# Kernel optimization log

Hardware: AMD Instinct MI355X
Metric: run time of the kernel (lower is better)

## Reference

```python
import jax, jax.numpy as jnp
import numpy as np

N_S, N_T, E, B = 100000, 100000, 2000000, 10000
F_XS, F_XT, F_E, F_U = 10, 5, 10, 10


def setup_inputs() -> dict:
    key = jax.random.key(0)
    ks = jax.random.split(key, 8)
    return {
        "x_s": jax.random.normal(ks[0], (N_S, F_XS), dtype=jnp.float32),
        "x_t": jax.random.normal(ks[1], (N_T, F_XT), dtype=jnp.float32),
        "edge_index": jax.random.randint(ks[2], (2, E), 0, N_S),
        "edge_attr": jax.random.normal(ks[3], (E, F_E), dtype=jnp.float32),
        "u": jax.random.normal(ks[4], (B, F_U), dtype=jnp.float32),
        "batch_e": jax.random.randint(ks[5], (E,), 0, B),
        "W1": jax.random.normal(ks[6], (F_XS + F_XT + F_E + F_U, F_E), dtype=jnp.float32) * (1.0 / np.sqrt(F_XS + F_XT + F_E + F_U)),
        "b1": jnp.zeros((F_E,), dtype=jnp.float32),
        "W2": jax.random.normal(ks[7], (F_E, F_E), dtype=jnp.float32) * (1.0 / np.sqrt(F_E)),
        "b2": jnp.zeros((F_E,), dtype=jnp.float32),
    }


def reference(x_s, x_t, edge_index, edge_attr, u, batch_e, W1, b1, W2, b2):
    src, tgt = edge_index[0], edge_index[1]
    # Gather + concat: [E, F_xs + F_xt + F_e + F_u]
    h = jnp.concatenate([x_s[src], x_t[tgt], edge_attr, u[batch_e]], axis=-1)
    h = jax.nn.leaky_relu(h @ W1 + b1, negative_slope=0.1)
    return h @ W2 + b2  # [E, F_e]
```

## Files before the change

kernel.cpp:

```cpp
#include <hip/hip_runtime.h>


#define F_XS 10
#define F_XT 5
#define F_E  10
#define F_U  10
#define F_IN 35

__global__ __launch_bounds__(256) void edge_model_kernel(
    const float* __restrict__ x_s,
    const float* __restrict__ x_t,
    const int*   __restrict__ edge_index,
    const float* __restrict__ edge_attr,
    const float* __restrict__ u,
    const int*   __restrict__ batch_e,
    const float* __restrict__ W1,
    const float* __restrict__ b1,
    const float* __restrict__ W2,
    const float* __restrict__ b2,
    float*       __restrict__ out,
    int E)
{
    const int e = blockIdx.x * blockDim.x + threadIdx.x;
    if (e >= E) return;

    const int src = edge_index[e];
    const int tgt = edge_index[E + e];
    const int be  = batch_e[e];

    float in[F_IN];

    {
        const float2* p = (const float2*)(x_s + (long long)src * F_XS);
        #pragma unroll
        for (int i = 0; i < 5; ++i) { float2 v = p[i]; in[2*i] = v.x; in[2*i+1] = v.y; }
    }
    {
        const float* p = x_t + (long long)tgt * F_XT;
        #pragma unroll
        for (int i = 0; i < 5; ++i) in[10 + i] = p[i];
    }
    {
        const float2* p = (const float2*)(edge_attr + (long long)e * F_E);
        #pragma unroll
        for (int i = 0; i < 5; ++i) { float2 v = p[i]; in[15 + 2*i] = v.x; in[16 + 2*i] = v.y; }
    }
    {
        const float2* p = (const float2*)(u + (long long)be * F_U);
        #pragma unroll
        for (int i = 0; i < 5; ++i) { float2 v = p[i]; in[25 + 2*i] = v.x; in[26 + 2*i] = v.y; }
    }

    float h[F_E];
    #pragma unroll
    for (int j = 0; j < F_E; ++j) h[j] = b1[j];
    #pragma unroll
    for (int k = 0; k < F_IN; ++k) {
        const float a = in[k];
        #pragma unroll
        for (int j = 0; j < F_E; ++j) h[j] = fmaf(a, W1[k * F_E + j], h[j]);
    }
    #pragma unroll
    for (int j = 0; j < F_E; ++j) h[j] = (h[j] >= 0.0f) ? h[j] : 0.1f * h[j];

    float o[F_E];
    #pragma unroll
    for (int j = 0; j < F_E; ++j) o[j] = b2[j];
    #pragma unroll
    for (int k = 0; k < F_E; ++k) {
        const float a = h[k];
        #pragma unroll
        for (int j = 0; j < F_E; ++j) o[j] = fmaf(a, W2[k * F_E + j], o[j]);
    }

    float2* po = (float2*)(out + (long long)e * F_E);
    #pragma unroll
    for (int i = 0; i < 5; ++i) {
        float2 v; v.x = o[2*i]; v.y = o[2*i + 1];
        po[i] = v;
    }
}

extern "C" void kernel_launch(void* const* d_in, const int* in_sizes, int n_in,
                              void* d_out, int out_size, void* d_ws, size_t ws_size,
                              hipStream_t stream) {
    const float* x_s        = (const float*)d_in[0];
    const float* x_t        = (const float*)d_in[1];
    const int*   edge_index = (const int*)  d_in[2];
    const float* edge_attr  = (const float*)d_in[3];
    const float* u          = (const float*)d_in[4];
    const int*   batch_e    = (const int*)  d_in[5];
    const float* W1         = (const float*)d_in[6];
    const float* b1         = (const float*)d_in[7];
    const float* W2         = (const float*)d_in[8];
    const float* b2         = (const float*)d_in[9];
    float*       out        = (float*)d_out;

    const int E = in_sizes[5];
    const int block = 256;
    const int grid  = (E + block - 1) / block;

    edge_model_kernel<<<grid, block, 0, stream>>>(
        x_s, x_t, edge_index, edge_attr, u, batch_e, W1, b1, W2, b2, out, E);
}
```

Measured before the change: 248.9 us.

## Process two edges per thread with wide vector gathers and nontemporal streaming

Each thread now handles a pair of adjacent edges. Index loads become int2, node and global-feature rows are gathered with float4/float2 loads, and edge_attr and the output use 16-byte nontemporal loads and stores since the pair's 80-byte span is aligned. The aim is fewer, wider memory transactions, more loads in flight per thread, and less cache pollution from streamed data. In exchange, register pressure roughly doubles, and float4 loads on 20- and 40-byte row strides rely on the hardware tolerating unaligned vector accesses.

New measurement: 276.1 us. 1.11x slower.

```diff
diff --git a/kernel.cpp b/kernel.cpp
--- a/kernel.cpp
+++ b/kernel.cpp
@@ -6,6 +6,50 @@
 #define F_E  10
 #define F_U  10
 #define F_IN 35
+
+typedef float vf4 __attribute__((ext_vector_type(4)));
+union F4 { vf4 v; float f[4]; };
+
+__device__ __forceinline__ void gather10(const float* __restrict__ p, float* __restrict__ dst) {
+    float4 a = *(const float4*)(p);
+    float4 b = *(const float4*)(p + 4);
+    float2 c = *(const float2*)(p + 8);
+    dst[0]=a.x; dst[1]=a.y; dst[2]=a.z; dst[3]=a.w;
+    dst[4]=b.x; dst[5]=b.y; dst[6]=b.z; dst[7]=b.w;
+    dst[8]=c.x; dst[9]=c.y;
+}
+
+__device__ __forceinline__ void gather5(const float* __restrict__ p, float* __restrict__ dst) {
+    float4 a = *(const float4*)(p);
+    dst[0]=a.x; dst[1]=a.y; dst[2]=a.z; dst[3]=a.w;
+    dst[4]=p[4];
+}
+
+__device__ __forceinline__ void mlp(const float* __restrict__ in,
+                                    const float* __restrict__ W1, const float* __restrict__ b1,
+                                    const float* __restrict__ W2, const float* __restrict__ b2,
+                                    float* __restrict__ o) {
+    float h[F_E];
+    #pragma unroll
+    for (int j = 0; j < F_E; ++j) h[j] = b1[j];
+    #pragma unroll
+    for (int k = 0; k < F_IN; ++k) {
+        const float a = in[k];
+        #pragma unroll
+        for (int j = 0; j < F_E; ++j) h[j] = fmaf(a, W1[k * F_E + j], h[j]);
+    }
+    #pragma unroll
+    for (int j = 0; j < F_E; ++j) h[j] = (h[j] >= 0.0f) ? h[j] : 0.1f * h[j];
+
+    #pragma unroll
+    for (int j = 0; j < F_E; ++j) o[j] = b2[j];
+    #pragma unroll
+    for (int k = 0; k < F_E; ++k) {
+        const float a = h[k];
+        #pragma unroll
+        for (int j = 0; j < F_E; ++j) o[j] = fmaf(a, W2[k * F_E + j], o[j]);
+    }
+}
 
 __global__ __launch_bounds__(256) void edge_model_kernel(
     const float* __restrict__ x_s,
@@ -21,63 +65,62 @@
     float*       __restrict__ out,
     int E)
 {
-    const int e = blockIdx.x * blockDim.x + threadIdx.x;
-    if (e >= E) return;
+    const int t  = blockIdx.x * blockDim.x + threadIdx.x;
+    const int e0 = 2 * t;
+    if (e0 >= E) return;
+    const bool two = (e0 + 1) < E;
 
-    const int src = edge_index[e];
-    const int tgt = edge_index[E + e];
-    const int be  = batch_e[e];
+    const int2 sp = *(const int2*)(edge_index + e0);
+    const int2 tp = *(const int2*)(edge_index + E + e0);
+    const int2 bp = *(const int2*)(batch_e + e0);
 
-    float in[F_IN];
+    float in0[F_IN], in1[F_IN];
+
+    gather10(x_s + (long long)sp.x * F_XS, in0);
+    gather5 (x_t + (long long)tp.x * F_XT, in0 + 10);
+    gather10(u   + (long long)bp.x * F_U,  in0 + 25);
+    if (two) {
+        gather10(x_s + (long long)sp.y * F_XS, in1);
+        gather5 (x_t + (long long)tp.y * F_XT, in1 + 10);
+        gather10(u   + (long long)bp.y * F_U,  in1 + 25);
+    }
 
     {
-        const float2* p = (const float2*)(x_s + (long long)src * F_XS);
+        const vf4* p = (const vf4*)(edge_attr + (long long)e0 * F_E);
+        F4 q[5];
+        if (two) {
+            #pragma unroll
+            for (int i = 0; i < 5; ++i) q[i].v = __builtin_nontemporal_load(p + i);
+        } else {
+            const float* ps = (const float*)p;
+            #pragma unroll
+            for (int i = 0; i < 10; ++i) ((float*)q)[i] = ps[i];
+        }
+        const float* qs = (const float*)q;
         #pragma unroll
-        for (int i = 0; i < 5; ++i) { float2 v = p[i]; in[2*i] = v.x; in[2*i+1] = v.y; }
-    }
-    {
-        const float* p = x_t + (long long)tgt * F_XT;
-        #pragma unroll
-        for (int i = 0; i < 5; ++i) in[10 + i] = p[i];
-    }
-    {
-        const float2* p = (const float2*)(edge_attr + (long long)e * F_E);
-        #pragma unroll
-        for (int i = 0; i < 5; ++i) { float2 v = p[i]; in[15 + 2*i] = v.x; in[16 + 2*i] = v.y; }
-    }
-    {
-        const float2* p = (const float2*)(u + (long long)be * F_U);
-        #pragma unroll
-        for (int i = 0; i < 5; ++i) { float2 v = p[i]; in[25 + 2*i] = v.x; in[26 + 2*i] = v.y; }
+        for (int i = 0; i < 10; ++i) { in0[15 + i] = qs[i]; }
+        if (two) {
+            #pragma unroll
+            for (int i = 0; i < 10; ++i) { in1[15 + i] = qs[10 + i]; }
+        }
     }
 
-    float h[F_E];
-    #pragma unroll
-    for (int j = 0; j < F_E; ++j) h[j] = b1[j];
-    #pragma unroll
-    for (int k = 0; k < F_IN; ++k) {
-        const float a = in[k];
+    float o0[F_E], o1[F_E];
+    mlp(in0, W1, b1, W2, b2, o0);
+    if (two) mlp(in1, W1, b1, W2, b2, o1);
+
+    if (two) {
+        F4 r[5];
+        float* rs = (float*)r;
         #pragma unroll
-        for (int j = 0; j < F_E; ++j) h[j] = fmaf(a, W1[k * F_E + j], h[j]);
-    }
-    #pragma unroll
-    for (int j = 0; j < F_E; ++j) h[j] = (h[j] >= 0.0f) ? h[j] : 0.1f * h[j];
-
-    float o[F_E];
-    #pragma unroll
-    for (int j = 0; j < F_E; ++j) o[j] = b2[j];
-    #pragma unroll
-    for (int k = 0; k < F_E; ++k) {
-        const float a = h[k];
+        for (int i = 0; i < 10; ++i) { rs[i] = o0[i]; rs[10 + i] = o1[i]; }
+        vf4* po = (vf4*)(out + (long long)e0 * F_E);
         #pragma unroll
-        for (int j = 0; j < F_E; ++j) o[j] = fmaf(a, W2[k * F_E + j], o[j]);
-    }
-
-    float2* po = (float2*)(out + (long long)e * F_E);
-    #pragma unroll
-    for (int i = 0; i < 5; ++i) {
-        float2 v; v.x = o[2*i]; v.y = o[2*i + 1];
-        po[i] = v;
+        for (int i = 0; i < 5; ++i) __builtin_nontemporal_store(r[i].v, po + i);
+    } else {
+        float* po = out + (long long)e0 * F_E;
+        #pragma unroll
+        for (int i = 0; i < 10; ++i) po[i] = o0[i];
     }
 }
 
@@ -97,8 +140,9 @@
     float*       out        = (float*)d_out;
 
     const int E = in_sizes[5];
+    const int nthreads = (E + 1) / 2;
     const int block = 256;
-    const int grid  = (E + block - 1) / block;
+    const int grid  = (nthreads + block - 1) / block;
 
     edge_model_kernel<<<grid, block, 0, stream>>>(
         x_s, x_t, edge_index, edge_attr, u, batch_e, W1, b1, W2, b2, out, E);
```
